# Optimization experiments

Measured on AMD Instinct MI355X. Metric: run time of the kernel, lower is better.

The kernel has to match this reference:

```python
import jax, jax.numpy as jnp
from jax import lax
import numpy as np

W = 64  # window_size

def setup_inputs() -> dict:
    key = jax.random.key(0)
    x = jax.random.normal(key, (262144, 32), dtype=jnp.float32)
    return {"x": x}

def _roll(x, init, op):
    # sliding window of size W along axis 0, stride 1, VALID -> (T-W+1, F)
    return lax.reduce_window(x, init, op, window_dimensions=(W, 1),
                             window_strides=(1, 1), padding="VALID")

def reference(x):
    # drop_na=True, stride=1, keep_original=False,
    # statistics = [mean, std, min, max, sum] concatenated on last axis.
    s = _roll(x, jnp.float32(0), lax.add)          # rolling sum
    s2 = _roll(x * x, jnp.float32(0), lax.add)     # rolling sum of squares
    mean = s / W
    # tf.math.reduce_std is population std: sqrt(E[x^2] - E[x]^2)
    std = jnp.sqrt(jnp.maximum(s2 / W - mean * mean, 0.0))
    mn = _roll(x, jnp.float32(jnp.inf), lax.min)
    mx = _roll(x, jnp.float32(-jnp.inf), lax.max)
    return jnp.concatenate([mean, std, mn, mx, s], axis=-1)
```

## Files before the change

kernel.cpp:

```cpp
#include <hip/hip_runtime.h>
#include <math.h>


#define WINW 64
#define RCH 16
#define NF 32

__global__ __launch_bounds__(256, 4) void rolling_stats_kernel(
    const float* __restrict__ x, float* __restrict__ out, int N, int T_out,
    int blocks_per_xcd) {
  int b = blockIdx.x;
  int xcd = b & 7;
  int idx = b >> 3;
  int vb = xcd * blocks_per_xcd + idx;

  int tid = vb * blockDim.x + (int)threadIdx.x;
  int c = tid & (NF - 1);
  int chunk = tid >> 5;
  int nchunk = (T_out + RCH - 1) / RCH;
  if (chunk >= nchunk) return;
  int t0 = chunk * RCH;

  const float* p = x + (size_t)t0 * NF + c;

  float smin[RCH], smax[RCH];
  float ssum = 0.f, ssq = 0.f;
  float rmin = INFINITY, rmax = -INFINITY;

#pragma unroll 16
  for (int j = WINW - 1; j >= RCH; --j) {
    float a = p[j * NF];
    rmin = fminf(rmin, a);
    rmax = fmaxf(rmax, a);
    ssum += a;
    ssq = fmaf(a, a, ssq);
  }
#pragma unroll
  for (int j = RCH - 1; j >= 0; --j) {
    float a = p[j * NF];
    rmin = fminf(rmin, a);
    rmax = fmaxf(rmax, a);
    ssum += a;
    ssq = fmaf(a, a, ssq);
    smin[j] = rmin;
    smax[j] = rmax;
  }

  float pmin = INFINITY, pmax = -INFINITY;
  float wsum = ssum, wsq = ssq;
  float* o = out + (size_t)t0 * (5 * NF) + c;
#pragma unroll
  for (int j = 0; j < RCH; ++j) {
    if (j > 0) {
      int rnew = t0 + (WINW - 1) + j;
      rnew = rnew < N ? rnew : N - 1;
      float bnew = x[(size_t)rnew * NF + c];
      float aold = p[(j - 1) * NF];
      pmin = fminf(pmin, bnew);
      pmax = fmaxf(pmax, bnew);
      wsum += bnew - aold;
      wsq = fmaf(bnew, bnew, wsq);
      wsq = fmaf(-aold, aold, wsq);
    }
    if (t0 + j < T_out) {
      float wmin = fminf(smin[j], pmin);
      float wmax = fmaxf(smax[j], pmax);
      float mean = wsum * 0.015625f;
      float var = fmaf(-mean, mean, wsq * 0.015625f);
      var = fmaxf(var, 0.f);
      float sd = sqrtf(var);
      float* orow = o + (size_t)j * (5 * NF);
      __builtin_nontemporal_store(mean, &orow[0 * NF]);
      __builtin_nontemporal_store(sd, &orow[1 * NF]);
      __builtin_nontemporal_store(wmin, &orow[2 * NF]);
      __builtin_nontemporal_store(wmax, &orow[3 * NF]);
      __builtin_nontemporal_store(wsum, &orow[4 * NF]);
    }
  }
}

extern "C" void kernel_launch(void* const* d_in, const int* in_sizes, int n_in,
                              void* d_out, int out_size, void* d_ws,
                              size_t ws_size, hipStream_t stream) {
  const float* x = (const float*)d_in[0];
  float* out = (float*)d_out;
  int N = in_sizes[0] / NF;
  int T_out = N - (WINW - 1);
  int nchunk = (T_out + RCH - 1) / RCH;
  int nthreads = nchunk * NF;
  int nblocks = (nthreads + 255) / 256;
  int nblocks_pad = (nblocks + 7) & ~7;
  int blocks_per_xcd = nblocks_pad >> 3;
  rolling_stats_kernel<<<nblocks_pad, 256, 0, stream>>>(x, out, N, T_out,
                                                        blocks_per_xcd);
}
```

Measured before the change: 196.3 us.

## Stage input rows in shared memory and drop XCD remap and nontemporal stores

Each block now loads its 128 output rows plus a 64-row halo into LDS with float4 coalesced loads, and all window reads come from LDS instead of repeated global loads. The XCD-aware block remapping is removed, and output stores become regular stores instead of nontemporal ones. The goal is to cut redundant global and L2 traffic from overlapping windows. The cost is 24KB of LDS per block, a barrier, and possibly worse cache behaviour for the large output write stream.

```diff
diff --git a/kernel.cpp b/kernel.cpp
--- a/kernel.cpp
+++ b/kernel.cpp
@@ -5,31 +5,40 @@
 #define WINW 64
 #define RCH 16
 #define NF 32
+#define CHUNKS_PER_BLK 8
+#define ROWS_PER_BLK (CHUNKS_PER_BLK * RCH)
+#define STAGE_ROWS (ROWS_PER_BLK + WINW)
 
 __global__ __launch_bounds__(256, 4) void rolling_stats_kernel(
-    const float* __restrict__ x, float* __restrict__ out, int N, int T_out,
-    int blocks_per_xcd) {
-  int b = blockIdx.x;
-  int xcd = b & 7;
-  int idx = b >> 3;
-  int vb = xcd * blocks_per_xcd + idx;
+    const float* __restrict__ x, float* __restrict__ out, int N, int T_out) {
+  __shared__ float tile[STAGE_ROWS * NF];
 
-  int tid = vb * blockDim.x + (int)threadIdx.x;
-  int c = tid & (NF - 1);
-  int chunk = tid >> 5;
-  int nchunk = (T_out + RCH - 1) / RCH;
-  if (chunk >= nchunk) return;
-  int t0 = chunk * RCH;
+  int t0_blk = blockIdx.x * ROWS_PER_BLK;
 
-  const float* p = x + (size_t)t0 * NF + c;
+  const float4* xv = (const float4*)x;
+  float4* tv = (float4*)tile;
+#pragma unroll
+  for (int it = 0; it < (STAGE_ROWS * NF / 4) / 256; ++it) {
+    int f = it * 256 + (int)threadIdx.x;
+    int r = f >> 3;
+    int gr = t0_blk + r;
+    gr = gr < N ? gr : N - 1;
+    tv[f] = xv[(size_t)gr * (NF / 4) + (f & 7)];
+  }
+  __syncthreads();
+
+  int c = (int)threadIdx.x & (NF - 1);
+  int lr0 = ((int)threadIdx.x >> 5) * RCH;
+  int t0 = t0_blk + lr0;
+  const float* tc = tile + c;
 
   float smin[RCH], smax[RCH];
   float ssum = 0.f, ssq = 0.f;
   float rmin = INFINITY, rmax = -INFINITY;
 
-#pragma unroll 16
+#pragma unroll
   for (int j = WINW - 1; j >= RCH; --j) {
-    float a = p[j * NF];
+    float a = tc[(lr0 + j) * NF];
     rmin = fminf(rmin, a);
     rmax = fmaxf(rmax, a);
     ssum += a;
@@ -37,7 +46,7 @@
   }
 #pragma unroll
   for (int j = RCH - 1; j >= 0; --j) {
-    float a = p[j * NF];
+    float a = tc[(lr0 + j) * NF];
     rmin = fminf(rmin, a);
     rmax = fmaxf(rmax, a);
     ssum += a;
@@ -52,10 +61,8 @@
 #pragma unroll
   for (int j = 0; j < RCH; ++j) {
     if (j > 0) {
-      int rnew = t0 + (WINW - 1) + j;
-      rnew = rnew < N ? rnew : N - 1;
-      float bnew = x[(size_t)rnew * NF + c];
-      float aold = p[(j - 1) * NF];
+      float bnew = tc[(lr0 + WINW - 1 + j) * NF];
+      float aold = tc[(lr0 + j - 1) * NF];
       pmin = fminf(pmin, bnew);
       pmax = fmaxf(pmax, bnew);
       wsum += bnew - aold;
@@ -70,11 +77,11 @@
       var = fmaxf(var, 0.f);
       float sd = sqrtf(var);
       float* orow = o + (size_t)j * (5 * NF);
-      __builtin_nontemporal_store(mean, &orow[0 * NF]);
-      __builtin_nontemporal_store(sd, &orow[1 * NF]);
-      __builtin_nontemporal_store(wmin, &orow[2 * NF]);
-      __builtin_nontemporal_store(wmax, &orow[3 * NF]);
-      __builtin_nontemporal_store(wsum, &orow[4 * NF]);
+      orow[0 * NF] = mean;
+      orow[1 * NF] = sd;
+      orow[2 * NF] = wmin;
+      orow[3 * NF] = wmax;
+      orow[4 * NF] = wsum;
     }
   }
 }
@@ -86,11 +93,6 @@
   float* out = (float*)d_out;
   int N = in_sizes[0] / NF;
   int T_out = N - (WINW - 1);
-  int nchunk = (T_out + RCH - 1) / RCH;
-  int nthreads = nchunk * NF;
-  int nblocks = (nthreads + 255) / 256;
-  int nblocks_pad = (nblocks + 7) & ~7;
-  int blocks_per_xcd = nblocks_pad >> 3;
-  rolling_stats_kernel<<<nblocks_pad, 256, 0, stream>>>(x, out, N, T_out,
-                                                        blocks_per_xcd);
+  int nblocks = (T_out + ROWS_PER_BLK - 1) / ROWS_PER_BLK;
+  rolling_stats_kernel<<<nblocks, 256, 0, stream>>>(x, out, N, T_out);
 }
```

New measurement: 185.1 us. -5.7%, faster.
